# Kernel optimization log

Measured on AMD Instinct MI355X. Metric: run time of the kernel, lower is better.

## Reference

```python
import jax, jax.numpy as jnp
import numpy as np

TOP_K = 2


def layer_norm(x, g, b, eps=1e-5):
    m = jnp.mean(x, axis=-1, keepdims=True)
    v = jnp.mean((x - m) ** 2, axis=-1, keepdims=True)
    return (x - m) * jax.lax.rsqrt(v + eps) * g + b


def setup_inputs() -> dict:
    key = jax.random.key(0)
    ks = jax.random.split(key, 6)
    B, P, D, E, K = 8, 1024, 1024, 8, TOP_K
    x = jax.random.normal(ks[0], (B, P, D), dtype=jnp.float32)
    noise = jax.random.normal(ks[1], (B * P * K, D), dtype=jnp.float32) * 1e-5
    Wg = jax.random.normal(ks[2], (D, E), dtype=jnp.float32) * 0.02
    bg = jnp.zeros((E,), dtype=jnp.float32)
    W1 = jax.random.normal(ks[3], (E, D, D), dtype=jnp.float32) * 0.02
    b1 = jnp.zeros((E, D), dtype=jnp.float32)
    W2 = jax.random.normal(ks[4], (E, D, D), dtype=jnp.float32) * 0.02
    b2 = jnp.zeros((E, D), dtype=jnp.float32)
    ln_g = jnp.ones((E, D), dtype=jnp.float32)
    ln_b = jnp.zeros((E, D), dtype=jnp.float32)
    gn_g = jnp.ones((D,), dtype=jnp.float32)
    gn_b = jnp.zeros((D,), dtype=jnp.float32)
    return {"x": x, "noise": noise, "Wg": Wg, "bg": bg, "W1": W1, "b1": b1,
            "W2": W2, "b2": b2, "ln_g": ln_g, "ln_b": ln_b, "gn_g": gn_g, "gn_b": gn_b}


def reference(x, noise, Wg, bg, W1, b1, W2, b2, ln_g, ln_b, gn_g, gn_b):
    # Eval-mode forward of Allocator (aux_loss == 0, not returned).
    B, P, D = x.shape
    E = Wg.shape[1]
    K = TOP_K
    N = B * P
    logits = jnp.einsum('bpd,de->bpe', x, Wg) + bg          # [B,P,E]
    probs = jax.nn.softmax(logits, axis=-1).reshape(N, E)
    _topk_probs, topk_idx = jax.lax.top_k(probs, K)          # probs unused in eval combine
    flat_idx = topk_idx.reshape(-1)                          # [N*K]
    sample_idx = jnp.repeat(jnp.arange(N), K)                # [N*K]
    batch_idx = sample_idx // P                              # [N*K]
    xg = x.reshape(N, D)[sample_idx] + noise                 # [N*K, D] gathered token copies
    sums = []
    for e in range(E):  # fixed small expert loop
        h = jax.nn.gelu(xg @ W1[e] + b1[e], approximate=False)
        y = h @ W2[e] + b2[e] + xg                           # Mlp + residual
        y = layer_norm(y, ln_g[e], ln_b[e])                  # Expert.norm
        m = (flat_idx == e)[:, None]
        # one_hot(batch_idx).T @ masked_output == per-batch segment sum (unweighted)
        sums.append(jax.ops.segment_sum(jnp.where(m, y, 0.0), batch_idx, num_segments=B))
    out = jnp.stack(sums, axis=0).transpose(1, 0, 2)         # [B, E, D]
    return layer_norm(out, gn_g, gn_b)
```

## Files before the change

### kernel.cpp

```cpp
#include <hip/hip_runtime.h>
#include <hip/hip_bf16.h>
#include <math.h>

#define D 1024
#define NTOK 8192
#define NSLOT 16384
#define NGRP 64
#define MAXTILE 136

typedef short bf16x8 __attribute__((ext_vector_type(8)));
typedef float floatx4 __attribute__((ext_vector_type(4)));

__device__ __forceinline__ unsigned short f2bf(float f) {
    __hip_bfloat16 h = __float2bfloat16(f);
    return *reinterpret_cast<unsigned short*>(&h);
}
__device__ __forceinline__ float bf2f(unsigned short u) {
    unsigned int v = ((unsigned int)u) << 16;
    return __uint_as_float(v);
}

__device__ __forceinline__ void load_lds16(const void* g, void* l) {
    __builtin_amdgcn_global_load_lds(
        (const __attribute__((address_space(1))) unsigned int*)g,
        (__attribute__((address_space(3))) unsigned int*)l, 16, 0, 0);
}

__global__ void zero_kernel(int* __restrict__ grp_cnt, float* __restrict__ S) {
    int i = blockIdx.x * 256 + threadIdx.x;
    if (i < NGRP) grp_cnt[i] = 0;
    if (i < 64 * D) S[i] = 0.f;
}

__global__ void route_kernel(const float* __restrict__ x, const float* __restrict__ Wg,
                             const float* __restrict__ bg, int* __restrict__ slot_e,
                             int* __restrict__ grp_cnt) {
    int wave = threadIdx.x >> 6;
    int lane = threadIdx.x & 63;
    int tok = blockIdx.x * 4 + wave;
    const float* xr = x + (size_t)tok * D;
    float acc[8] = {0.f,0.f,0.f,0.f,0.f,0.f,0.f,0.f};
    for (int k = lane; k < D; k += 64) {
        float xv = xr[k];
        const float4* w4 = reinterpret_cast<const float4*>(Wg + k * 8);
        float4 a = w4[0], b = w4[1];
        acc[0] += xv * a.x; acc[1] += xv * a.y; acc[2] += xv * a.z; acc[3] += xv * a.w;
        acc[4] += xv * b.x; acc[5] += xv * b.y; acc[6] += xv * b.z; acc[7] += xv * b.w;
    }
#pragma unroll
    for (int e = 0; e < 8; e++) {
#pragma unroll
        for (int off = 32; off > 0; off >>= 1)
            acc[e] += __shfl_xor(acc[e], off, 64);
    }
    if (lane == 0) {
        float lg[8];
#pragma unroll
        for (int e = 0; e < 8; e++) lg[e] = acc[e] + bg[e];
        int e1 = 0; float b1v = lg[0];
#pragma unroll
        for (int e = 1; e < 8; e++) if (lg[e] > b1v) { b1v = lg[e]; e1 = e; }
        int e2 = -1; float b2v = -3.0e38f;
#pragma unroll
        for (int e = 0; e < 8; e++) { if (e == e1) continue; if (lg[e] > b2v) { b2v = lg[e]; e2 = e; } }
        int b = tok >> 10;
        slot_e[2 * tok] = e1;
        slot_e[2 * tok + 1] = e2;
        atomicAdd(&grp_cnt[e1 * 8 + b], 1);
        atomicAdd(&grp_cnt[e2 * 8 + b], 1);
    }
}

__global__ void prefix_kernel(const int* __restrict__ grp_cnt, int* __restrict__ goff,
                              int* __restrict__ cursor, int2* __restrict__ tile_tab) {
    if (threadIdx.x != 0) return;
    int s = 0;
    for (int g = 0; g < NGRP; g++) { goff[g] = s; cursor[g] = s; s += grp_cnt[g]; }
    goff[NGRP] = s;
    int t = 0;
    for (int e = 0; e < 8; e++) {
        int cnt = goff[e * 8 + 8] - goff[e * 8];
        for (int m0 = 0; m0 < cnt; m0 += 128) tile_tab[t++] = make_int2(e, m0);
    }
    for (; t < MAXTILE; t++) tile_tab[t] = make_int2(-1, 0);
}

__global__ void build_xg_kernel(const float* __restrict__ x, const float* __restrict__ noise,
                                const int* __restrict__ slot_e, int* __restrict__ cursor,
                                unsigned short* __restrict__ xg) {
    int wave = threadIdx.x >> 6;
    int lane = threadIdx.x & 63;
    int slot = blockIdx.x * 4 + wave;
    int e = slot_e[slot];
    int b = slot >> 11;
    int row = 0;
    if (lane == 0) row = atomicAdd(&cursor[e * 8 + b], 1);
    row = __shfl(row, 0, 64);
    int tok = slot >> 1;
    const float4* xr = reinterpret_cast<const float4*>(x + (size_t)tok * D);
    const float4* nr = reinterpret_cast<const float4*>(noise + (size_t)slot * D);
    ushort4* og = reinterpret_cast<ushort4*>(xg + (size_t)row * D);
    for (int i = lane; i < D / 4; i += 64) {
        float4 a = xr[i], n = nr[i];
        ushort4 o;
        o.x = f2bf(a.x + n.x); o.y = f2bf(a.y + n.y);
        o.z = f2bf(a.z + n.z); o.w = f2bf(a.w + n.w);
        og[i] = o;
    }
}

__global__ void wconv_kernel(const float* __restrict__ W1, const float* __restrict__ W2,
                             unsigned short* __restrict__ W1t, unsigned short* __restrict__ W2t) {
    int z = blockIdx.y;
    int mat = z & 1, e = z >> 1;
    int kb = blockIdx.x;
    const float* src = (mat ? W2 : W1) + (size_t)e * D * D + (size_t)kb * 8 * D;
    unsigned short* dst = (mat ? W2t : W1t) + (size_t)e * D * D + (size_t)kb * (D * 8);
    int t = threadIdx.x;
    float4 v[8];
#pragma unroll
    for (int k = 0; k < 8; k++)
        v[k] = reinterpret_cast<const float4*>(src + (size_t)k * D)[t];
    const float* vf = reinterpret_cast<const float*>(v);
#pragma unroll
    for (int c = 0; c < 4; c++) {
        unsigned int w[4];
#pragma unroll
        for (int j = 0; j < 4; j++) {
            unsigned short lo = f2bf(vf[(2 * j) * 4 + c]);
            unsigned short hi = f2bf(vf[(2 * j + 1) * 4 + c]);
            w[j] = (unsigned int)lo | ((unsigned int)hi << 16);
        }
        *reinterpret_cast<uint4*>(dst + (size_t)(t * 4 + c) * 8) = make_uint4(w[0], w[1], w[2], w[3]);
    }
}

template <int MODE>
__global__ __launch_bounds__(256)
void gemm_kernel(const unsigned short* __restrict__ A,
                 const unsigned short* __restrict__ Wt,
                 const float* __restrict__ bias,
                 const unsigned short* __restrict__ xg,
                 const int2* __restrict__ tile_tab,
                 const int* __restrict__ goff,
                 unsigned short* __restrict__ Hout) {
    __shared__ unsigned short As[2][128 * 32];
    __shared__ unsigned short Bs[2][64 * 32];

    int id = blockIdx.x;
    int xcd = id & 7;
    int rem = id >> 3;
    int ntile = rem & 15;
    int t = xcd + 8 * (rem >> 4);
    int2 tt = tile_tab[t];
    int e = tt.x;
    if (e < 0) return;
    int m0 = tt.y;
    int rowBase = goff[e * 8];
    int cnt = goff[e * 8 + 8] - rowBase;
    int n0 = ntile * 64;

    int tid = threadIdx.x;
    int lane = tid & 63, wave = tid >> 6;
    int wm = wave >> 1, wn = wave & 1;
    int lr = lane & 15, quad = lane >> 4;
    int l2 = lane >> 2, l4 = lane & 3;

    int arow0 = min(m0 + (wave * 2 + 0) * 16 + l2, cnt - 1);
    int arow1 = min(m0 + (wave * 2 + 1) * 16 + l2, cnt - 1);
    const unsigned short* ap0 = A + ((size_t)(rowBase + arow0) << 10) + l4 * 8;
    const unsigned short* ap1 = A + ((size_t)(rowBase + arow1) << 10) + l4 * 8;
    const unsigned short* bp = Wt + (size_t)e * D * D
                               + (size_t)l4 * (D * 8)
                               + (size_t)(n0 + wave * 16 + l2) * 8;

    unsigned short* a_dst0[2] = { &As[0][(wave * 2 + 0) * 512 + lane * 8],
                                  &As[1][(wave * 2 + 0) * 512 + lane * 8] };
    unsigned short* a_dst1[2] = { &As[0][(wave * 2 + 1) * 512 + lane * 8],
                                  &As[1][(wave * 2 + 1) * 512 + lane * 8] };
    unsigned short* b_dst[2]  = { &Bs[0][wave * 512 + lane * 8],
                                  &Bs[1][wave * 512 + lane * 8] };

    const unsigned short* a_frag = &As[0][(wm * 64 + lr) * 32 + quad * 8];
    const unsigned short* b_frag = &Bs[0][(wn * 32 + lr) * 32 + quad * 8];

    floatx4 acc[4][2] = {};

    load_lds16(ap0, a_dst0[0]); load_lds16(ap1, a_dst1[0]); load_lds16(bp, b_dst[0]);
    ap0 += 32; ap1 += 32; bp += 4 * D * 8;

#pragma unroll 1
    for (int k0 = 0; k0 < D; k0 += 64) {
        __syncthreads();
        if (k0 + 32 < D) {
            load_lds16(ap0, a_dst0[1]); load_lds16(ap1, a_dst1[1]); load_lds16(bp, b_dst[1]);
            ap0 += 32; ap1 += 32; bp += 4 * D * 8;
        }
        {
            bf16x8 af[4], bfr[2];
#pragma unroll
            for (int i = 0; i < 4; i++)
                af[i] = *reinterpret_cast<const bf16x8*>(a_frag + i * 512);
#pragma unroll
            for (int j = 0; j < 2; j++)
                bfr[j] = *reinterpret_cast<const bf16x8*>(b_frag + j * 512);
#pragma unroll
            for (int i = 0; i < 4; i++)
#pragma unroll
                for (int j = 0; j < 2; j++)
                    acc[i][j] = __builtin_amdgcn_mfma_f32_16x16x32_bf16(af[i], bfr[j], acc[i][j], 0, 0, 0);
        }
        __syncthreads();
        if (k0 + 64 < D) {
            load_lds16(ap0, a_dst0[0]); load_lds16(ap1, a_dst1[0]); load_lds16(bp, b_dst[0]);
            ap0 += 32; ap1 += 32; bp += 4 * D * 8;
        }
        {
            bf16x8 af[4], bfr[2];
#pragma unroll
            for (int i = 0; i < 4; i++)
                af[i] = *reinterpret_cast<const bf16x8*>(a_frag + 4096 + i * 512);
#pragma unroll
            for (int j = 0; j < 2; j++)
                bfr[j] = *reinterpret_cast<const bf16x8*>(b_frag + 2048 + j * 512);
#pragma unroll
            for (int i = 0; i < 4; i++)
#pragma unroll
                for (int j = 0; j < 2; j++)
                    acc[i][j] = __builtin_amdgcn_mfma_f32_16x16x32_bf16(af[i], bfr[j], acc[i][j], 0, 0, 0);
        }
    }

#pragma unroll
    for (int i = 0; i < 4; i++) {
        int rowb = m0 + wm * 64 + i * 16 + quad * 4;
#pragma unroll
        for (int j = 0; j < 2; j++) {
            int col = n0 + wn * 32 + j * 16 + lr;
            float bia = bias[e * D + col];
#pragma unroll
            for (int r = 0; r < 4; r++) {
                int rr = rowb + r;
                if (rr < cnt) {
                    float v = acc[i][j][r] + bia;
                    size_t idx = (size_t)(rowBase + rr) * D + col;
                    if (MODE == 0) {
                        float g = 0.5f * v * (1.0f + erff(v * 0.70710678118654752f));
                        Hout[idx] = f2bf(g);
                    } else {
                        v += bf2f(xg[idx]);
                        Hout[idx] = f2bf(v);
                    }
                }
            }
        }
    }
}

__global__ void lnsum_kernel(const unsigned short* __restrict__ ybf,
                             const int* __restrict__ goff, float* __restrict__ S) {
    int grp = blockIdx.x, chunk = blockIdx.y;
    int r0 = goff[grp] + chunk * 64;
    int r1 = min(goff[grp + 1], r0 + 64);
    if (r0 >= r1) return;
    __shared__ float part[D];
    for (int i = threadIdx.x; i < D; i += 256) part[i] = 0.f;
    __syncthreads();

    int wave = threadIdx.x >> 6, lane = threadIdx.x & 63;
    float p[16] = {0.f};
    for (int r = r0 + wave; r < r1; r += 4) {
        const unsigned short* row = ybf + ((size_t)r << 10);
        float v[16];
        float s = 0.f, sq = 0.f;
#pragma unroll
        for (int c = 0; c < 4; c++) {
            ushort4 u = *reinterpret_cast<const ushort4*>(row + c * 256 + lane * 4);
            float a = bf2f(u.x), b = bf2f(u.y), cc = bf2f(u.z), d = bf2f(u.w);
            v[c * 4 + 0] = a; v[c * 4 + 1] = b; v[c * 4 + 2] = cc; v[c * 4 + 3] = d;
            s += a + b + cc + d;
            sq += a * a + b * b + cc * cc + d * d;
        }
#pragma unroll
        for (int off = 32; off > 0; off >>= 1) {
            s += __shfl_xor(s, off, 64);
            sq += __shfl_xor(sq, off, 64);
        }
        float m = s * (1.f / 1024.f);
        float rs = rsqrtf(sq * (1.f / 1024.f) - m * m + 1e-5f);
#pragma unroll
        for (int c = 0; c < 16; c++) p[c] += (v[c] - m) * rs;
    }
#pragma unroll
    for (int c = 0; c < 4; c++)
#pragma unroll
        for (int q = 0; q < 4; q++)
            atomicAdd(&part[c * 256 + lane * 4 + q], p[c * 4 + q]);
    __syncthreads();

    int e = grp >> 3, b = grp & 7;
    float* Sp = S + (size_t)(b * 8 + e) * D;
    for (int i = threadIdx.x; i < D; i += 256)
        atomicAdd(&Sp[i], part[i]);
}

__global__ void finalize_kernel(const float* __restrict__ S, const int* __restrict__ goff,
                                const float* __restrict__ ln_g, const float* __restrict__ ln_b,
                                const float* __restrict__ gn_g, const float* __restrict__ gn_b,
                                float* __restrict__ out) {
    int be = blockIdx.x;
    int b = be >> 3, e = be & 7;
    int grp = e * 8 + b;
    float cnt = (float)(goff[grp + 1] - goff[grp]);
    int tid = threadIdx.x;
    __shared__ float red[8];
    float val[4];
    float s = 0.f, sq = 0.f;
#pragma unroll
    for (int c = 0; c < 4; c++) {
        int d = tid * 4 + c;
        float v = S[(size_t)be * D + d] * ln_g[e * D + d] + cnt * ln_b[e * D + d];
        val[c] = v; s += v; sq += v * v;
    }
#pragma unroll
    for (int off = 32; off > 0; off >>= 1) {
        s += __shfl_xor(s, off, 64);
        sq += __shfl_xor(sq, off, 64);
    }
    int wave = tid >> 6, lane = tid & 63;
    if (lane == 0) { red[wave] = s; red[4 + wave] = sq; }
    __syncthreads();
    float ts = red[0] + red[1] + red[2] + red[3];
    float tq = red[4] + red[5] + red[6] + red[7];
    float m = ts / 1024.f;
    float var = tq / 1024.f - m * m;
    float rstd = rsqrtf(var + 1e-5f);
#pragma unroll
    for (int c = 0; c < 4; c++) {
        int d = tid * 4 + c;
        out[(size_t)be * D + d] = (val[c] - m) * rstd * gn_g[d] + gn_b[d];
    }
}

extern "C" void kernel_launch(void* const* d_in, const int* in_sizes, int n_in,
                              void* d_out, int out_size, void* d_ws, size_t ws_size,
                              hipStream_t stream) {
    const float* x     = (const float*)d_in[0];
    const float* noise = (const float*)d_in[1];
    const float* Wg    = (const float*)d_in[2];
    const float* bg    = (const float*)d_in[3];
    const float* W1    = (const float*)d_in[4];
    const float* b1    = (const float*)d_in[5];
    const float* W2    = (const float*)d_in[6];
    const float* b2    = (const float*)d_in[7];
    const float* ln_g  = (const float*)d_in[8];
    const float* ln_b  = (const float*)d_in[9];
    const float* gn_g  = (const float*)d_in[10];
    const float* gn_b  = (const float*)d_in[11];
    float* out = (float*)d_out;

    char* ws = (char*)d_ws;
    size_t off = 0;
    unsigned short* xg   = (unsigned short*)(ws + off); off += (size_t)NSLOT * D * 2;
    unsigned short* hb   = (unsigned short*)(ws + off); off += (size_t)NSLOT * D * 2;
    unsigned short* ybf  = (unsigned short*)(ws + off); off += (size_t)NSLOT * D * 2;
    unsigned short* W1t  = (unsigned short*)(ws + off); off += (size_t)8 * D * D * 2;
    unsigned short* W2t  = (unsigned short*)(ws + off); off += (size_t)8 * D * D * 2;
    int* slot_e          = (int*)(ws + off);            off += (size_t)NSLOT * 4;
    int* grp_cnt         = (int*)(ws + off);            off += 256;
    int* goff            = (int*)(ws + off);            off += 512;
    int* cursor          = (int*)(ws + off);            off += 256;
    int2* tile_tab       = (int2*)(ws + off);           off += MAXTILE * 8;
    float* S             = (float*)(ws + off);          off += (size_t)64 * D * 4;

    zero_kernel<<<256, 256, 0, stream>>>(grp_cnt, S);
    route_kernel<<<NTOK / 4, 256, 0, stream>>>(x, Wg, bg, slot_e, grp_cnt);
    prefix_kernel<<<1, 64, 0, stream>>>(grp_cnt, goff, cursor, tile_tab);
    wconv_kernel<<<dim3(128, 16), 256, 0, stream>>>(W1, W2, W1t, W2t);
    build_xg_kernel<<<NSLOT / 4, 256, 0, stream>>>(x, noise, slot_e, cursor, xg);
    gemm_kernel<0><<<dim3(2176), 256, 0, stream>>>(xg, W1t, b1, xg, tile_tab, goff, hb);
    gemm_kernel<1><<<dim3(2176), 256, 0, stream>>>(hb, W2t, b2, xg, tile_tab, goff, ybf);
    lnsum_kernel<<<dim3(64, 32), 256, 0, stream>>>(ybf, goff, S);
    finalize_kernel<<<64, 256, 0, stream>>>(S, goff, ln_g, ln_b, gn_g, gn_b, out);
}
```

Measured before the change: 538.6 us.

## Replace LDS-staged expert GEMM with register-direct 64x256 tiles

```diff
diff --git a/kernel.cpp b/kernel.cpp
--- a/kernel.cpp
+++ b/kernel.cpp
@@ -6,7 +6,7 @@
 #define NTOK 8192
 #define NSLOT 16384
 #define NGRP 64
-#define MAXTILE 136
+#define MAXT64 272
 
 typedef short bf16x8 __attribute__((ext_vector_type(8)));
 typedef float floatx4 __attribute__((ext_vector_type(4)));
@@ -18,12 +18,6 @@
 __device__ __forceinline__ float bf2f(unsigned short u) {
     unsigned int v = ((unsigned int)u) << 16;
     return __uint_as_float(v);
-}
-
-__device__ __forceinline__ void load_lds16(const void* g, void* l) {
-    __builtin_amdgcn_global_load_lds(
-        (const __attribute__((address_space(1))) unsigned int*)g,
-        (__attribute__((address_space(3))) unsigned int*)l, 16, 0, 0);
 }
 
 __global__ void zero_kernel(int* __restrict__ grp_cnt, float* __restrict__ S) {
@@ -72,7 +66,7 @@
 }
 
 __global__ void prefix_kernel(const int* __restrict__ grp_cnt, int* __restrict__ goff,
-                              int* __restrict__ cursor, int2* __restrict__ tile_tab) {
+                              int* __restrict__ cursor, int2* __restrict__ tile64) {
     if (threadIdx.x != 0) return;
     int s = 0;
     for (int g = 0; g < NGRP; g++) { goff[g] = s; cursor[g] = s; s += grp_cnt[g]; }
@@ -80,9 +74,9 @@
     int t = 0;
     for (int e = 0; e < 8; e++) {
         int cnt = goff[e * 8 + 8] - goff[e * 8];
-        for (int m0 = 0; m0 < cnt; m0 += 128) tile_tab[t++] = make_int2(e, m0);
-    }
-    for (; t < MAXTILE; t++) tile_tab[t] = make_int2(-1, 0);
+        for (int m0 = 0; m0 < cnt; m0 += 64) tile64[t++] = make_int2(e, m0);
+    }
+    for (; t < MAXT64; t++) tile64[t] = make_int2(-1, 0);
 }
 
 __global__ void build_xg_kernel(const float* __restrict__ x, const float* __restrict__ noise,
@@ -141,109 +135,77 @@
                  const unsigned short* __restrict__ Wt,
                  const float* __restrict__ bias,
                  const unsigned short* __restrict__ xg,
-                 const int2* __restrict__ tile_tab,
+                 const int2* __restrict__ tile64,
                  const int* __restrict__ goff,
                  unsigned short* __restrict__ Hout) {
-    __shared__ unsigned short As[2][128 * 32];
-    __shared__ unsigned short Bs[2][64 * 32];
-
     int id = blockIdx.x;
     int xcd = id & 7;
-    int rem = id >> 3;
-    int ntile = rem & 15;
-    int t = xcd + 8 * (rem >> 4);
-    int2 tt = tile_tab[t];
+    int seq = id >> 3;
+    int nb = seq / 34;
+    int mseq = seq - nb * 34;
+    int2 tt = tile64[mseq * 8 + xcd];
     int e = tt.x;
     if (e < 0) return;
     int m0 = tt.y;
     int rowBase = goff[e * 8];
     int cnt = goff[e * 8 + 8] - rowBase;
-    int n0 = ntile * 64;
-
-    int tid = threadIdx.x;
-    int lane = tid & 63, wave = tid >> 6;
-    int wm = wave >> 1, wn = wave & 1;
+
+    int lane = threadIdx.x & 63, wave = threadIdx.x >> 6;
     int lr = lane & 15, quad = lane >> 4;
-    int l2 = lane >> 2, l4 = lane & 3;
-
-    int arow0 = min(m0 + (wave * 2 + 0) * 16 + l2, cnt - 1);
-    int arow1 = min(m0 + (wave * 2 + 1) * 16 + l2, cnt - 1);
-    const unsigned short* ap0 = A + ((size_t)(rowBase + arow0) << 10) + l4 * 8;
-    const unsigned short* ap1 = A + ((size_t)(rowBase + arow1) << 10) + l4 * 8;
-    const unsigned short* bp = Wt + (size_t)e * D * D
-                               + (size_t)l4 * (D * 8)
-                               + (size_t)(n0 + wave * 16 + l2) * 8;
-
-    unsigned short* a_dst0[2] = { &As[0][(wave * 2 + 0) * 512 + lane * 8],
-                                  &As[1][(wave * 2 + 0) * 512 + lane * 8] };
-    unsigned short* a_dst1[2] = { &As[0][(wave * 2 + 1) * 512 + lane * 8],
-                                  &As[1][(wave * 2 + 1) * 512 + lane * 8] };
-    unsigned short* b_dst[2]  = { &Bs[0][wave * 512 + lane * 8],
-                                  &Bs[1][wave * 512 + lane * 8] };
-
-    const unsigned short* a_frag = &As[0][(wm * 64 + lr) * 32 + quad * 8];
-    const unsigned short* b_frag = &Bs[0][(wn * 32 + lr) * 32 + quad * 8];
-
-    floatx4 acc[4][2] = {};
-
-    load_lds16(ap0, a_dst0[0]); load_lds16(ap1, a_dst1[0]); load_lds16(bp, b_dst[0]);
-    ap0 += 32; ap1 += 32; bp += 4 * D * 8;
+    int n0 = nb * 256 + wave * 64;
+
+    const unsigned short* ap = A + (((size_t)(rowBase + m0 + lr)) << 10) + quad * 8;
+    const unsigned short* bp = Wt + ((size_t)e << 20) + (size_t)quad * 8192 + (size_t)(n0 + lr) * 8;
+
+    floatx4 acc[4][4] = {};
+    bf16x8 a0[4], b0[4], a1[4], b1[4];
+
+#pragma unroll
+    for (int i = 0; i < 4; i++) a0[i] = *reinterpret_cast<const bf16x8*>(ap + i * 16384);
+#pragma unroll
+    for (int j = 0; j < 4; j++) b0[j] = *reinterpret_cast<const bf16x8*>(bp + j * 128);
 
 #pragma unroll 1
     for (int k0 = 0; k0 < D; k0 += 64) {
-        __syncthreads();
-        if (k0 + 32 < D) {
-            load_lds16(ap0, a_dst0[1]); load_lds16(ap1, a_dst1[1]); load_lds16(bp, b_dst[1]);
-            ap0 += 32; ap1 += 32; bp += 4 * D * 8;
-        }
-        {
-            bf16x8 af[4], bfr[2];
-#pragma unroll
-            for (int i = 0; i < 4; i++)
-                af[i] = *reinterpret_cast<const bf16x8*>(a_frag + i * 512);
-#pragma unroll
-            for (int j = 0; j < 2; j++)
-                bfr[j] = *reinterpret_cast<const bf16x8*>(b_frag + j * 512);
-#pragma unroll
-            for (int i = 0; i < 4; i++)
-#pragma unroll
-                for (int j = 0; j < 2; j++)
-                    acc[i][j] = __builtin_amdgcn_mfma_f32_16x16x32_bf16(af[i], bfr[j], acc[i][j], 0, 0, 0);
-        }
-        __syncthreads();
+        const unsigned short* apn = ap + (k0 + 32);
+        const unsigned short* bpn = bp + ((size_t)(k0 + 32) << 10);
+#pragma unroll
+        for (int i = 0; i < 4; i++) a1[i] = *reinterpret_cast<const bf16x8*>(apn + i * 16384);
+#pragma unroll
+        for (int j = 0; j < 4; j++) b1[j] = *reinterpret_cast<const bf16x8*>(bpn + j * 128);
+#pragma unroll
+        for (int i = 0; i < 4; i++)
+#pragma unroll
+            for (int j = 0; j < 4; j++)
+                acc[i][j] = __builtin_amdgcn_mfma_f32_16x16x32_bf16(a0[i], b0[j], acc[i][j], 0, 0, 0);
         if (k0 + 64 < D) {
-            load_lds16(ap0, a_dst0[0]); load_lds16(ap1, a_dst1[0]); load_lds16(bp, b_dst[0]);
-            ap0 += 32; ap1 += 32; bp += 4 * D * 8;
-        }
-        {
-            bf16x8 af[4], bfr[2];
-#pragma unroll
-            for (int i = 0; i < 4; i++)
-                af[i] = *reinterpret_cast<const bf16x8*>(a_frag + 4096 + i * 512);
-#pragma unroll
-            for (int j = 0; j < 2; j++)
-                bfr[j] = *reinterpret_cast<const bf16x8*>(b_frag + 2048 + j * 512);
-#pragma unroll
-            for (int i = 0; i < 4; i++)
-#pragma unroll
-                for (int j = 0; j < 2; j++)
-                    acc[i][j] = __builtin_amdgcn_mfma_f32_16x16x32_bf16(af[i], bfr[j], acc[i][j], 0, 0, 0);
-        }
+            const unsigned short* apm = ap + (k0 + 64);
+            const unsigned short* bpm = bp + ((size_t)(k0 + 64) << 10);
+#pragma unroll
+            for (int i = 0; i < 4; i++) a0[i] = *reinterpret_cast<const bf16x8*>(apm + i * 16384);
+#pragma unroll
+            for (int j = 0; j < 4; j++) b0[j] = *reinterpret_cast<const bf16x8*>(bpm + j * 128);
+        }
+#pragma unroll
+        for (int i = 0; i < 4; i++)
+#pragma unroll
+            for (int j = 0; j < 4; j++)
+                acc[i][j] = __builtin_amdgcn_mfma_f32_16x16x32_bf16(a1[i], b1[j], acc[i][j], 0, 0, 0);
     }
 
 #pragma unroll
     for (int i = 0; i < 4; i++) {
-        int rowb = m0 + wm * 64 + i * 16 + quad * 4;
-#pragma unroll
-        for (int j = 0; j < 2; j++) {
-            int col = n0 + wn * 32 + j * 16 + lr;
+        int rowb = m0 + i * 16 + quad * 4;
+#pragma unroll
+        for (int j = 0; j < 4; j++) {
+            int col = n0 + j * 16 + lr;
             float bia = bias[e * D + col];
 #pragma unroll
             for (int r = 0; r < 4; r++) {
                 int rr = rowb + r;
                 if (rr < cnt) {
                     float v = acc[i][j][r] + bia;
-                    size_t idx = (size_t)(rowBase + rr) * D + col;
+                    size_t idx = (((size_t)(rowBase + rr)) << 10) + col;
                     if (MODE == 0) {
                         float g = 0.5f * v * (1.0f + erff(v * 0.70710678118654752f));
                         Hout[idx] = f2bf(g);
@@ -260,8 +222,8 @@
 __global__ void lnsum_kernel(const unsigned short* __restrict__ ybf,
                              const int* __restrict__ goff, float* __restrict__ S) {
     int grp = blockIdx.x, chunk = blockIdx.y;
-    int r0 = goff[grp] + chunk * 64;
-    int r1 = min(goff[grp + 1], r0 + 64);
+    int r0 = goff[grp] + chunk * 128;
+    int r1 = min(goff[grp + 1], r0 + 128);
     if (r0 >= r1) return;
     __shared__ float part[D];
     for (int i = threadIdx.x; i < D; i += 256) part[i] = 0.f;
@@ -370,16 +332,16 @@
     int* grp_cnt         = (int*)(ws + off);            off += 256;
     int* goff            = (int*)(ws + off);            off += 512;
     int* cursor          = (int*)(ws + off);            off += 256;
-    int2* tile_tab       = (int2*)(ws + off);           off += MAXTILE * 8;
+    int2* tile64         = (int2*)(ws + off);           off += MAXT64 * 8;
     float* S             = (float*)(ws + off);          off += (size_t)64 * D * 4;
 
     zero_kernel<<<256, 256, 0, stream>>>(grp_cnt, S);
     route_kernel<<<NTOK / 4, 256, 0, stream>>>(x, Wg, bg, slot_e, grp_cnt);
-    prefix_kernel<<<1, 64, 0, stream>>>(grp_cnt, goff, cursor, tile_tab);
+    prefix_kernel<<<1, 64, 0, stream>>>(grp_cnt, goff, cursor, tile64);
     wconv_kernel<<<dim3(128, 16), 256, 0, stream>>>(W1, W2, W1t, W2t);
     build_xg_kernel<<<NSLOT / 4, 256, 0, stream>>>(x, noise, slot_e, cursor, xg);
-    gemm_kernel<0><<<dim3(2176), 256, 0, stream>>>(xg, W1t, b1, xg, tile_tab, goff, hb);
-    gemm_kernel<1><<<dim3(2176), 256, 0, stream>>>(hb, W2t, b2, xg, tile_tab, goff, ybf);
-    lnsum_kernel<<<dim3(64, 32), 256, 0, stream>>>(ybf, goff, S);
+    gemm_kernel<0><<<dim3(1088), 256, 0, stream>>>(xg, W1t, b1, xg, tile64, goff, hb);
+    gemm_kernel<1><<<dim3(1088), 256, 0, stream>>>(hb, W2t, b2, xg, tile64, goff, ybf);
+    lnsum_kernel<<<dim3(64, 16), 256, 0, stream>>>(ybf, goff, S);
     finalize_kernel<<<64, 256, 0, stream>>>(S, goff, ln_g, ln_b, gn_g, gn_b, out);
 }
```

Result: slower. 656.0 us (+21.8%).
